# Performance work log

Measured on AMD Instinct MI355X. Metric: run time of the kernel, lower is better.

The kernel has to match this reference:

```python
import jax, jax.numpy as jnp
import numpy as np

VOCAB, E, H, L, B, T = 32000, 64, 8, 25, 1000, 512


def setup_inputs() -> dict:
    key = jax.random.key(0)
    ks = jax.random.split(key, 6)
    return {
        "x": jax.random.randint(ks[0], (B, T), 0, VOCAB),
        "h_0": jnp.zeros((L, B, H), jnp.float32),
        "embedding": jax.random.normal(ks[1], (VOCAB, E), jnp.float32) * 0.02,
        "W_xh0": jax.random.normal(ks[2], (E, H), jnp.float32) / np.float32(np.sqrt(E)),
        "W_xh_rest": jax.random.normal(ks[3], (L - 1, H, H), jnp.float32) / np.float32(np.sqrt(H)),
        "W_hh": jax.random.normal(ks[4], (L, H, H), jnp.float32) / np.float32(np.sqrt(H)),
        "b_h": jnp.zeros((L, H), jnp.float32),
        "W_hy": jax.random.normal(ks[5], (H, 1), jnp.float32) / np.float32(np.sqrt(H)),
        "b_y": jnp.zeros((1,), jnp.float32),
    }


def reference(x, h_0, embedding, W_xh0, W_xh_rest, W_hh, b_h, W_hy, b_y):
    # x: [B, T] int ids; embedded: [B, T, E]
    emb = embedding[x]
    n_layers = h_0.shape[0]

    def step(h, e_t):  # h: [L, B, H], e_t: [B, E]
        inp = e_t
        hs = []
        for i in range(n_layers):  # fixed small layer count -> unrolled
            W = W_xh0 if i == 0 else W_xh_rest[i - 1]
            h_i = jnp.tanh(inp @ W + h[i] @ W_hh[i] + b_h[i])
            hs.append(h_i)
            inp = h_i
        return jnp.stack(hs, 0), None

    h_last, _ = jax.lax.scan(step, h_0, jnp.swapaxes(emb, 0, 1))  # scan over time
    logits = h_last[-1] @ W_hy + b_y  # [B, 1]
    return logits.squeeze(1), h_last
```

## Files before the change

kernel.cpp:

```cpp
#include <hip/hip_runtime.h>

#define VOCAB 32000
#define E 64
#define H 8
#define L 25
#define B 1000
#define T 512

#define CHUNK 8
#define NCHUNK (T / CHUNK)
#define NSTEP (NCHUNK + L - 1)
#define BPB 2
#define THREADS 448

#define LAYER_STRIDE 132
#define BLOC_STRIDE (L * LAYER_STRIDE)
#define LDS_FLOATS (BPB * BLOC_STRIDE)

__global__ __launch_bounds__(256) void proj_kernel(
    const float* __restrict__ emb, const float* __restrict__ w0,
    float* __restrict__ ptab)
{
    int gid = blockIdx.x * 256 + threadIdx.x;
    if (gid >= VOCAB * H) return;
    int j = gid & 7;
    int r = gid >> 3;
    const float* e = emb + r * E;
    float a0 = 0.f, a1 = 0.f, a2 = 0.f, a3 = 0.f;
#pragma unroll
    for (int k = 0; k < E; k += 4) {
        a0 += e[k + 0] * w0[(k + 0) * H + j];
        a1 += e[k + 1] * w0[(k + 1) * H + j];
        a2 += e[k + 2] * w0[(k + 2) * H + j];
        a3 += e[k + 3] * w0[(k + 3) * H + j];
    }
    ptab[gid] = (a0 + a1) + (a2 + a3);
}

__device__ __forceinline__ float fast_tanh(float x) {
    float e2 = __expf(2.0f * x);
    return 1.0f - 2.0f / (e2 + 1.0f);
}

__global__ __launch_bounds__(THREADS) void rnn_recur(
    const int*   __restrict__ x,
    const float* __restrict__ h0,
    const float* __restrict__ wrest,
    const float* __restrict__ whh_g,
    const float* __restrict__ bh,
    const float* __restrict__ why,
    const float* __restrict__ by,
    const float* __restrict__ ptab,
    float*       __restrict__ out)
{
    __shared__ __align__(16) float buf[LDS_FLOATS];

    const int tid = threadIdx.x;
    for (int k = tid; k < LDS_FLOATS; k += THREADS) buf[k] = 0.f;

    const int bloc = tid / 200;
    const int r    = tid - bloc * 200;
    const int i    = r >> 3;
    const int j    = r & 7;
    const bool active = (tid < BPB * 200);
    const int b = blockIdx.x * BPB + bloc;

    float wx[8], whh[8];
    float bias = 0.f, hj = 0.f;
    float* mybuf = &buf[(bloc < BPB ? bloc : 0) * BLOC_STRIDE + i * LAYER_STRIDE];
    const float* prevbuf = mybuf - LAYER_STRIDE;

    if (active) {
#pragma unroll
        for (int k = 0; k < 8; ++k) {
            whh[k] = whh_g[(i * 8 + k) * 8 + j];
            wx[k]  = (i > 0) ? wrest[((i - 1) * 8 + k) * 8 + j] : 0.f;
        }
        bias = bh[i * 8 + j];
        hj = h0[(i * B + b) * H + j];
    }
    __syncthreads();
    if (active) {
        mybuf[1 * (CHUNK * 8) + (CHUNK - 1) * 8 + j] = hj;
    }
    __syncthreads();

    const int xbase = b * T;

    for (int s = 0; s < NSTEP; ++s) {
        const int c = s - i;
        if (active && (unsigned)c < (unsigned)NCHUNK) {
            const int p  = c & 1;
            const int t0 = c * CHUNK;
            float* wptr = mybuf + p * (CHUNK * 8);
            const float* hp0 = mybuf + (p ^ 1) * (CHUNK * 8) + (CHUNK - 1) * 8;

            float4 ha = *(const float4*)hp0;
            float4 hb = *(const float4*)(hp0 + 4);

            if (i == 0) {
                int tok[CHUNK];
#pragma unroll
                for (int ct = 0; ct < CHUNK; ++ct) tok[ct] = x[xbase + t0 + ct];
                float pv[CHUNK];
#pragma unroll
                for (int ct = 0; ct < CHUNK; ++ct) pv[ct] = ptab[tok[ct] * H + j];
#pragma unroll
                for (int ct = 0; ct < CHUNK; ++ct) {
                    float a0 = pv[ct] + bias;
                    float a1 = ha.y * whh[1];
                    float a2 = ha.z * whh[2];
                    float a3 = ha.w * whh[3];
                    a0 += ha.x * whh[0];
                    a1 += hb.x * whh[4];
                    a2 += hb.y * whh[5];
                    a3 += hb.z * whh[6];
                    a0 += hb.w * whh[7];
                    float hn = fast_tanh((a0 + a1) + (a2 + a3));
                    wptr[ct * 8 + j] = hn;
                    hj = hn;
                    __builtin_amdgcn_wave_barrier();
                    ha = *(const float4*)(wptr + ct * 8);
                    hb = *(const float4*)(wptr + ct * 8 + 4);
                }
            } else {
                const float* iptr = prevbuf + p * (CHUNK * 8);
#pragma unroll
                for (int ct = 0; ct < CHUNK; ++ct) {
                    float4 ia = *(const float4*)(iptr + ct * 8);
                    float4 ib = *(const float4*)(iptr + ct * 8 + 4);
                    float a0 = bias      + ia.x * wx[0];
                    float a1 = ia.y * wx[1] + ia.z * wx[2];
                    float a2 = ia.w * wx[3] + ib.x * wx[4];
                    float a3 = ib.y * wx[5] + ib.z * wx[6];
                    a0 += ib.w * wx[7];
                    a1 += ha.x * whh[0];
                    a2 += ha.y * whh[1];
                    a3 += ha.z * whh[2];
                    a0 += ha.w * whh[3];
                    a1 += hb.x * whh[4];
                    a2 += hb.y * whh[5];
                    a3 += hb.z * whh[6];
                    a0 += hb.w * whh[7];
                    float hn = fast_tanh((a0 + a1) + (a2 + a3));
                    wptr[ct * 8 + j] = hn;
                    hj = hn;
                    __builtin_amdgcn_wave_barrier();
                    ha = *(const float4*)(wptr + ct * 8);
                    hb = *(const float4*)(wptr + ct * 8 + 4);
                }
            }

            if (c == NCHUNK - 1) {
                out[B + (i * B + b) * H + j] = hj;
                if (i == L - 1) {
                    float part = hj * why[j];
                    part += __shfl_xor(part, 1, 8);
                    part += __shfl_xor(part, 2, 8);
                    part += __shfl_xor(part, 4, 8);
                    if (j == 0) out[b] = part + by[0];
                }
            }
        }
        __syncthreads();
    }
}

extern "C" void kernel_launch(void* const* d_in, const int* in_sizes, int n_in,
                              void* d_out, int out_size, void* d_ws, size_t ws_size,
                              hipStream_t stream) {
    const int*   x     = (const int*)d_in[0];
    const float* h0    = (const float*)d_in[1];
    const float* emb   = (const float*)d_in[2];
    const float* w0    = (const float*)d_in[3];
    const float* wrest = (const float*)d_in[4];
    const float* whh   = (const float*)d_in[5];
    const float* bh    = (const float*)d_in[6];
    const float* why   = (const float*)d_in[7];
    const float* by    = (const float*)d_in[8];
    float* out  = (float*)d_out;
    float* ptab = (float*)d_ws;

    hipLaunchKernelGGL(proj_kernel, dim3((VOCAB * H + 255) / 256), dim3(256),
                       0, stream, emb, w0, ptab);
    hipLaunchKernelGGL(rnn_recur, dim3(B / BPB), dim3(THREADS),
                       0, stream, x, h0, wrest, whh, bh, why, by, ptab, out);
}
```

Before: 276.2 us.

## Use one batch row per block and DPP lane exchange for recurrent state

Each block now handles one batch element with 256 threads instead of two per 448-thread block. Within a layer's 8-lane group, the hidden state is exchanged through DPP/swizzle lane permutations rather than LDS round trips, and the math uses packed 2-wide float vectors. Layer-0 token and projection loads are prefetched one chunk ahead. The projection kernel stages W0 in LDS and reads embeddings as float4. The 8-lane in-register exchange shortens the serial per-timestep dependency chain, at the cost of more blocks, each doing less work.

```diff
diff --git a/kernel.cpp b/kernel.cpp
--- a/kernel.cpp
+++ b/kernel.cpp
@@ -10,29 +10,36 @@
 #define CHUNK 8
 #define NCHUNK (T / CHUNK)
 #define NSTEP (NCHUNK + L - 1)
-#define BPB 2
-#define THREADS 448
+#define THREADS 256
 
 #define LAYER_STRIDE 132
-#define BLOC_STRIDE (L * LAYER_STRIDE)
-#define LDS_FLOATS (BPB * BLOC_STRIDE)
+#define LDS_FLOATS (L * LAYER_STRIDE)
+
+typedef float v2f __attribute__((ext_vector_type(2)));
 
 __global__ __launch_bounds__(256) void proj_kernel(
     const float* __restrict__ emb, const float* __restrict__ w0,
     float* __restrict__ ptab)
 {
-    int gid = blockIdx.x * 256 + threadIdx.x;
+    __shared__ float w0s[E * H];
+    int tid = threadIdx.x;
+    w0s[tid] = w0[tid];
+    w0s[tid + 256] = w0[tid + 256];
+    __syncthreads();
+
+    int gid = blockIdx.x * 256 + tid;
     if (gid >= VOCAB * H) return;
     int j = gid & 7;
     int r = gid >> 3;
-    const float* e = emb + r * E;
+    const float4* e4 = (const float4*)(emb + r * E);
     float a0 = 0.f, a1 = 0.f, a2 = 0.f, a3 = 0.f;
 #pragma unroll
-    for (int k = 0; k < E; k += 4) {
-        a0 += e[k + 0] * w0[(k + 0) * H + j];
-        a1 += e[k + 1] * w0[(k + 1) * H + j];
-        a2 += e[k + 2] * w0[(k + 2) * H + j];
-        a3 += e[k + 3] * w0[(k + 3) * H + j];
+    for (int k4 = 0; k4 < E / 4; ++k4) {
+        float4 v = e4[k4];
+        a0 += v.x * w0s[(4 * k4 + 0) * H + j];
+        a1 += v.y * w0s[(4 * k4 + 1) * H + j];
+        a2 += v.z * w0s[(4 * k4 + 2) * H + j];
+        a3 += v.w * w0s[(4 * k4 + 3) * H + j];
     }
     ptab[gid] = (a0 + a1) + (a2 + a3);
 }
@@ -40,6 +47,16 @@
 __device__ __forceinline__ float fast_tanh(float x) {
     float e2 = __expf(2.0f * x);
     return 1.0f - 2.0f / (e2 + 1.0f);
+}
+
+__device__ __forceinline__ float fxor1(float x) {
+    return __int_as_float(__builtin_amdgcn_mov_dpp(__float_as_int(x), 0xB1, 0xF, 0xF, true));
+}
+__device__ __forceinline__ float fxor2(float x) {
+    return __int_as_float(__builtin_amdgcn_mov_dpp(__float_as_int(x), 0x4E, 0xF, 0xF, true));
+}
+__device__ __forceinline__ float fxor4(float x) {
+    return __int_as_float(__builtin_amdgcn_ds_swizzle(__float_as_int(x), 0x101F));
 }
 
 __global__ __launch_bounds__(THREADS) void rnn_recur(
@@ -56,109 +73,118 @@
     __shared__ __align__(16) float buf[LDS_FLOATS];
 
     const int tid = threadIdx.x;
-    for (int k = tid; k < LDS_FLOATS; k += THREADS) buf[k] = 0.f;
-
-    const int bloc = tid / 200;
-    const int r    = tid - bloc * 200;
-    const int i    = r >> 3;
-    const int j    = r & 7;
-    const bool active = (tid < BPB * 200);
-    const int b = blockIdx.x * BPB + bloc;
-
-    float wx[8], whh[8];
-    float bias = 0.f, hj = 0.f;
-    float* mybuf = &buf[(bloc < BPB ? bloc : 0) * BLOC_STRIDE + i * LAYER_STRIDE];
+    const int i = tid >> 3;
+    const int j = tid & 7;
+    const bool active = tid < L * H;
+    const int b = blockIdx.x;
+
+    v2f wh01 = {0.f, 0.f}, wh23 = {0.f, 0.f}, wh45 = {0.f, 0.f}, wh67 = {0.f, 0.f};
+    v2f wx01 = {0.f, 0.f}, wx23 = {0.f, 0.f}, wx45 = {0.f, 0.f}, wx67 = {0.f, 0.f};
+    v2f h01  = {0.f, 0.f}, h23  = {0.f, 0.f}, h45  = {0.f, 0.f}, h67  = {0.f, 0.f};
+    float bias = 0.f, byv = 0.f;
+    float wy0 = 0.f, wy1 = 0.f, wy2 = 0.f, wy3 = 0.f,
+          wy4 = 0.f, wy5 = 0.f, wy6 = 0.f, wy7 = 0.f;
+
+    float* mybuf = &buf[i * LAYER_STRIDE];
     const float* prevbuf = mybuf - LAYER_STRIDE;
 
     if (active) {
-#pragma unroll
-        for (int k = 0; k < 8; ++k) {
-            whh[k] = whh_g[(i * 8 + k) * 8 + j];
-            wx[k]  = (i > 0) ? wrest[((i - 1) * 8 + k) * 8 + j] : 0.f;
+        const float* whL = whh_g + i * 64;
+        wh01 = (v2f){whL[(j ^ 0) * 8 + j], whL[(j ^ 1) * 8 + j]};
+        wh23 = (v2f){whL[(j ^ 2) * 8 + j], whL[(j ^ 3) * 8 + j]};
+        wh45 = (v2f){whL[(j ^ 4) * 8 + j], whL[(j ^ 5) * 8 + j]};
+        wh67 = (v2f){whL[(j ^ 6) * 8 + j], whL[(j ^ 7) * 8 + j]};
+        if (i > 0) {
+            const float* wxL = wrest + (i - 1) * 64;
+            wx01 = (v2f){wxL[0 * 8 + j], wxL[1 * 8 + j]};
+            wx23 = (v2f){wxL[2 * 8 + j], wxL[3 * 8 + j]};
+            wx45 = (v2f){wxL[4 * 8 + j], wxL[5 * 8 + j]};
+            wx67 = (v2f){wxL[6 * 8 + j], wxL[7 * 8 + j]};
         }
         bias = bh[i * 8 + j];
-        hj = h0[(i * B + b) * H + j];
-    }
-    __syncthreads();
-    if (active) {
-        mybuf[1 * (CHUNK * 8) + (CHUNK - 1) * 8 + j] = hj;
-    }
-    __syncthreads();
+        const float* h0p = h0 + (i * B + b) * H;
+        h01 = (v2f){h0p[j ^ 0], h0p[j ^ 1]};
+        h23 = (v2f){h0p[j ^ 2], h0p[j ^ 3]};
+        h45 = (v2f){h0p[j ^ 4], h0p[j ^ 5]};
+        h67 = (v2f){h0p[j ^ 6], h0p[j ^ 7]};
+        if (i == L - 1) {
+            wy0 = why[j ^ 0]; wy1 = why[j ^ 1]; wy2 = why[j ^ 2]; wy3 = why[j ^ 3];
+            wy4 = why[j ^ 4]; wy5 = why[j ^ 5]; wy6 = why[j ^ 6]; wy7 = why[j ^ 7];
+            byv = by[0];
+        }
+    }
 
     const int xbase = b * T;
+    float pv[CHUNK];
+    if (active && i == 0) {
+#pragma unroll
+        for (int ct = 0; ct < CHUNK; ++ct)
+            pv[ct] = ptab[x[xbase + ct] * H + j];
+    }
 
     for (int s = 0; s < NSTEP; ++s) {
         const int c = s - i;
         if (active && (unsigned)c < (unsigned)NCHUNK) {
-            const int p  = c & 1;
-            const int t0 = c * CHUNK;
+            const int p = c & 1;
             float* wptr = mybuf + p * (CHUNK * 8);
-            const float* hp0 = mybuf + (p ^ 1) * (CHUNK * 8) + (CHUNK - 1) * 8;
-
-            float4 ha = *(const float4*)hp0;
-            float4 hb = *(const float4*)(hp0 + 4);
-
-            if (i == 0) {
-                int tok[CHUNK];
-#pragma unroll
-                for (int ct = 0; ct < CHUNK; ++ct) tok[ct] = x[xbase + t0 + ct];
-                float pv[CHUNK];
-#pragma unroll
-                for (int ct = 0; ct < CHUNK; ++ct) pv[ct] = ptab[tok[ct] * H + j];
-#pragma unroll
-                for (int ct = 0; ct < CHUNK; ++ct) {
-                    float a0 = pv[ct] + bias;
-                    float a1 = ha.y * whh[1];
-                    float a2 = ha.z * whh[2];
-                    float a3 = ha.w * whh[3];
-                    a0 += ha.x * whh[0];
-                    a1 += hb.x * whh[4];
-                    a2 += hb.y * whh[5];
-                    a3 += hb.z * whh[6];
-                    a0 += hb.w * whh[7];
-                    float hn = fast_tanh((a0 + a1) + (a2 + a3));
-                    wptr[ct * 8 + j] = hn;
-                    hj = hn;
-                    __builtin_amdgcn_wave_barrier();
-                    ha = *(const float4*)(wptr + ct * 8);
-                    hb = *(const float4*)(wptr + ct * 8 + 4);
-                }
-            } else {
-                const float* iptr = prevbuf + p * (CHUNK * 8);
-#pragma unroll
-                for (int ct = 0; ct < CHUNK; ++ct) {
+            const float* iptr = prevbuf + p * (CHUNK * 8);
+
+            int tokn[CHUNK];
+            const bool pf = (i == 0) && (c + 1 < NCHUNK);
+            if (pf) {
+#pragma unroll
+                for (int ct = 0; ct < CHUNK; ++ct)
+                    tokn[ct] = x[xbase + (c + 1) * CHUNK + ct];
+            }
+
+#pragma unroll
+            for (int ct = 0; ct < CHUNK; ++ct) {
+                v2f acc, acc2;
+                if (i == 0) {
+                    acc  = (v2f){pv[ct] + bias, 0.f};
+                    acc2 = (v2f){0.f, 0.f};
+                } else {
                     float4 ia = *(const float4*)(iptr + ct * 8);
                     float4 ib = *(const float4*)(iptr + ct * 8 + 4);
-                    float a0 = bias      + ia.x * wx[0];
-                    float a1 = ia.y * wx[1] + ia.z * wx[2];
-                    float a2 = ia.w * wx[3] + ib.x * wx[4];
-                    float a3 = ib.y * wx[5] + ib.z * wx[6];
-                    a0 += ib.w * wx[7];
-                    a1 += ha.x * whh[0];
-                    a2 += ha.y * whh[1];
-                    a3 += ha.z * whh[2];
-                    a0 += ha.w * whh[3];
-                    a1 += hb.x * whh[4];
-                    a2 += hb.y * whh[5];
-                    a3 += hb.z * whh[6];
-                    a0 += hb.w * whh[7];
-                    float hn = fast_tanh((a0 + a1) + (a2 + a3));
-                    wptr[ct * 8 + j] = hn;
-                    hj = hn;
-                    __builtin_amdgcn_wave_barrier();
-                    ha = *(const float4*)(wptr + ct * 8);
-                    hb = *(const float4*)(wptr + ct * 8 + 4);
+                    acc   = (v2f){bias, 0.f};
+                    acc  += (v2f){ia.x, ia.y} * wx01;
+                    acc2  = (v2f){ia.z, ia.w} * wx23;
+                    acc  += (v2f){ib.x, ib.y} * wx45;
+                    acc2 += (v2f){ib.z, ib.w} * wx67;
                 }
+                acc  += h01 * wh01;
+                acc2 += h23 * wh23;
+                acc  += h45 * wh45;
+                acc2 += h67 * wh67;
+                v2f at = acc + acc2;
+                float hn = fast_tanh(at.x + at.y);
+
+                if (i < L - 1) wptr[ct * 8 + j] = hn;
+
+                float o1 = fxor1(hn);
+                float p0 = fxor2(hn);
+                float p1 = fxor2(o1);
+                h01 = (v2f){hn, o1};
+                h23 = (v2f){p0, p1};
+                h45 = (v2f){fxor4(hn), fxor4(o1)};
+                h67 = (v2f){fxor4(p0), fxor4(p1)};
+            }
+
+            if (pf) {
+#pragma unroll
+                for (int ct = 0; ct < CHUNK; ++ct)
+                    pv[ct] = ptab[tokn[ct] * H + j];
             }
 
             if (c == NCHUNK - 1) {
-                out[B + (i * B + b) * H + j] = hj;
+                out[B + (i * B + b) * H + j] = h01.x;
                 if (i == L - 1) {
-                    float part = hj * why[j];
-                    part += __shfl_xor(part, 1, 8);
-                    part += __shfl_xor(part, 2, 8);
-                    part += __shfl_xor(part, 4, 8);
-                    if (j == 0) out[b] = part + by[0];
+                    float lg = byv;
+                    lg += h01.x * wy0 + h01.y * wy1;
+                    lg += h23.x * wy2 + h23.y * wy3;
+                    lg += h45.x * wy4 + h45.y * wy5;
+                    lg += h67.x * wy6 + h67.y * wy7;
+                    if (j == 0) out[b] = lg;
                 }
             }
         }
@@ -183,6 +209,6 @@
 
     hipLaunchKernelGGL(proj_kernel, dim3((VOCAB * H + 255) / 256), dim3(256),
                        0, stream, emb, w0, ptab);
-    hipLaunchKernelGGL(rnn_recur, dim3(B / BPB), dim3(THREADS),
+    hipLaunchKernelGGL(rnn_recur, dim3(B), dim3(THREADS),
                        0, stream, x, h0, wrest, whh, bh, why, by, ptab, out);
 }
```

Result: no change. 271.9 us (-1.6%).
